# Performance work log

Hardware: AMD Instinct MI355X
Metric: run time of the kernel (lower is better)

Reference implementation:

```python
import jax, jax.numpy as jnp
import numpy as np

N = 16777216  # number of sample points
L = 2         # n_layers


def _layer_unitary(w):
    """U = RZ(w2) @ RY(w1) @ RX(w0), each a standard 2x2 rotation gate."""
    h = w * 0.5
    c, s = jnp.cos(h), jnp.sin(h)
    i = jnp.complex64(1j)
    rx = jnp.array([[1, 0], [0, 1]], jnp.complex64) * c[0] + jnp.array([[0, 1], [1, 0]], jnp.complex64) * (-i * s[0])
    ry = jnp.array([[c[1], -s[1]], [s[1], c[1]]], jnp.complex64)
    rz = jnp.array([[jnp.exp(-i * h[2]), 0.0 + 0.0j], [0.0 + 0.0j, jnp.exp(i * h[2])]], jnp.complex64)
    return rz @ ry @ rx


def setup_inputs() -> dict:
    key = jax.random.key(0)
    k1, k2 = jax.random.split(key)
    x = jax.random.normal(k1, (N, 1), dtype=jnp.float32)
    weights = 0.1 * jax.random.normal(k2, (L, 3), dtype=jnp.float32)
    a = jnp.asarray(1.0, jnp.float32)
    b = jnp.asarray(0.0, jnp.float32)
    return {"x": x, "weights": weights, "a": a, "b": b}


def reference(x, weights, a, b):
    # Total weight-only unitary: product over layers (applied layer 0 first).
    U = jnp.eye(2, dtype=jnp.complex64)
    for l in range(weights.shape[0]):  # static, tiny (L=2)
        U = _layer_unitary(weights[l]) @ U
    # RY(x)|0> = [cos(x/2), sin(x/2)]
    xh = 0.5 * x.reshape(-1)
    state0 = jnp.stack([jnp.cos(xh), jnp.sin(xh)], axis=-1).astype(jnp.complex64)  # [N,2]
    s = jnp.einsum('ij,nj->ni', U, state0)  # [N,2]
    z = (s[:, 0].real ** 2 + s[:, 0].imag ** 2) - (s[:, 1].real ** 2 + s[:, 1].imag ** 2)
    return a * z.reshape(-1, 1) + b
```

## Files before the change

### kernel.cpp

```cpp
#include <hip/hip_runtime.h>


struct cplx { float re, im; };

__device__ inline cplx cmul(cplx p, cplx q) {
    return cplx{p.re * q.re - p.im * q.im, p.re * q.im + p.im * q.re};
}
__device__ inline cplx cadd(cplx p, cplx q) { return cplx{p.re + q.re, p.im + q.im}; }

__device__ inline void qpinn_coeffs(const float* __restrict__ w, float a, float b,
                                    float& K0, float& K1, float& K2) {
    cplx U00{1.f, 0.f}, U01{0.f, 0.f}, U10{0.f, 0.f}, U11{1.f, 0.f};
    #pragma unroll
    for (int l = 0; l < 2; ++l) {
        const float h0 = 0.5f * w[3 * l + 0];
        const float h1 = 0.5f * w[3 * l + 1];
        const float h2 = 0.5f * w[3 * l + 2];
        float c0, s0, c1, s1, c2, s2;
        __sincosf(h0, &s0, &c0);
        __sincosf(h1, &s1, &c1);
        __sincosf(h2, &s2, &c2);

        cplx X00{c0, 0.f}, X01{0.f, -s0}, X10{0.f, -s0}, X11{c0, 0.f};
        cplx Y00{c1, 0.f}, Y01{-s1, 0.f}, Y10{s1, 0.f}, Y11{c1, 0.f};
        cplx A00 = cadd(cmul(Y00, X00), cmul(Y01, X10));
        cplx A01 = cadd(cmul(Y00, X01), cmul(Y01, X11));
        cplx A10 = cadd(cmul(Y10, X00), cmul(Y11, X10));
        cplx A11 = cadd(cmul(Y10, X01), cmul(Y11, X11));
        cplx zm{c2, -s2}, zp{c2, s2};
        cplx L00 = cmul(zm, A00), L01 = cmul(zm, A01);
        cplx L10 = cmul(zp, A10), L11 = cmul(zp, A11);
        cplx n00 = cadd(cmul(L00, U00), cmul(L01, U10));
        cplx n01 = cadd(cmul(L00, U01), cmul(L01, U11));
        cplx n10 = cadd(cmul(L10, U00), cmul(L11, U10));
        cplx n11 = cadd(cmul(L10, U01), cmul(L11, U11));
        U00 = n00; U01 = n01; U10 = n10; U11 = n11;
    }
    const float A = (U00.re * U00.re + U00.im * U00.im) - (U10.re * U10.re + U10.im * U10.im);
    const float B = (U01.re * U01.re + U01.im * U01.im) - (U11.re * U11.re + U11.im * U11.im);
    const float C = 2.f * ((U00.re * U01.re + U00.im * U01.im) -
                           (U10.re * U11.re + U10.im * U11.im));
    K0 = fmaf(a, 0.5f * (A + B), b);
    K1 = a * 0.5f * (A - B);
    K2 = a * 0.5f * C;
}

__global__ __launch_bounds__(256) void qpinn_fused(
    const float* __restrict__ x, const float* __restrict__ w,
    const float* __restrict__ pa, const float* __restrict__ pb,
    float* __restrict__ out, int n4) {

    __shared__ float sc[3];
    if (threadIdx.x == 0) {
        float K0, K1, K2;
        qpinn_coeffs(w, pa[0], pb[0], K0, K1, K2);
        sc[0] = K0; sc[1] = K1; sc[2] = K2;
    }
    __syncthreads();
    const float K0 = sc[0];
    const float K1 = sc[1];
    const float K2 = sc[2];

    const float4* __restrict__ x4 = (const float4*)x;
    float4* __restrict__ o4 = (float4*)out;

    const int stride = gridDim.x * blockDim.x;
    for (int i = blockIdx.x * blockDim.x + threadIdx.x; i < n4; i += stride) {
        float4 v = x4[i];
        float4 r;
        float sx, cx;
        __sincosf(v.x, &sx, &cx); r.x = fmaf(K1, cx, fmaf(K2, sx, K0));
        __sincosf(v.y, &sx, &cx); r.y = fmaf(K1, cx, fmaf(K2, sx, K0));
        __sincosf(v.z, &sx, &cx); r.z = fmaf(K1, cx, fmaf(K2, sx, K0));
        __sincosf(v.w, &sx, &cx); r.w = fmaf(K1, cx, fmaf(K2, sx, K0));
        o4[i] = r;
    }
}

extern "C" void kernel_launch(void* const* d_in, const int* in_sizes, int n_in,
                              void* d_out, int out_size, void* d_ws, size_t ws_size,
                              hipStream_t stream) {
    const float* x = (const float*)d_in[0];
    const float* w = (const float*)d_in[1];
    const float* a = (const float*)d_in[2];
    const float* b = (const float*)d_in[3];
    float* out = (float*)d_out;

    const int n = in_sizes[0];
    const int n4 = n / 4;
    const int block = 256;
    const int grid = 2048;

    qpinn_fused<<<grid, block, 0, stream>>>(x, w, a, b, out, n4);
}
```

Measured before the change: 117.2 us.

## Fold sin/cos combination into single phase-shifted hardware cosine with nontemporal stores

Rewrites K1*cos(x)+K2*sin(x) as R*cos(x - phi), precomputing the amplitude and phase in revolutions so each element needs one v_cos instruction instead of a sincos pair. The grid-stride loop is also unrolled to handle two float4 vectors per iteration, and outputs use nontemporal stores. The kernel is memory-bound at this size, so the main gain would come from fewer ALU ops and better memory-level parallelism. Precision of the raw hardware cosine over larger arguments is a risk.

```diff
diff --git a/kernel.cpp b/kernel.cpp
--- a/kernel.cpp
+++ b/kernel.cpp
@@ -1,5 +1,7 @@
 #include <hip/hip_runtime.h>
 
+
+typedef float f32x4 __attribute__((ext_vector_type(4)));
 
 struct cplx { float re, im; };
 
@@ -9,7 +11,7 @@
 __device__ inline cplx cadd(cplx p, cplx q) { return cplx{p.re + q.re, p.im + q.im}; }
 
 __device__ inline void qpinn_coeffs(const float* __restrict__ w, float a, float b,
-                                    float& K0, float& K1, float& K2) {
+                                    float& K0, float& R, float& mphirev) {
     cplx U00{1.f, 0.f}, U01{0.f, 0.f}, U10{0.f, 0.f}, U11{1.f, 0.f};
     #pragma unroll
     for (int l = 0; l < 2; ++l) {
@@ -17,9 +19,9 @@
         const float h1 = 0.5f * w[3 * l + 1];
         const float h2 = 0.5f * w[3 * l + 2];
         float c0, s0, c1, s1, c2, s2;
-        __sincosf(h0, &s0, &c0);
-        __sincosf(h1, &s1, &c1);
-        __sincosf(h2, &s2, &c2);
+        sincosf(h0, &s0, &c0);
+        sincosf(h1, &s1, &c1);
+        sincosf(h2, &s2, &c2);
 
         cplx X00{c0, 0.f}, X01{0.f, -s0}, X10{0.f, -s0}, X11{c0, 0.f};
         cplx Y00{c1, 0.f}, Y01{-s1, 0.f}, Y10{s1, 0.f}, Y11{c1, 0.f};
@@ -41,8 +43,21 @@
     const float C = 2.f * ((U00.re * U01.re + U00.im * U01.im) -
                            (U10.re * U11.re + U10.im * U11.im));
     K0 = fmaf(a, 0.5f * (A + B), b);
-    K1 = a * 0.5f * (A - B);
-    K2 = a * 0.5f * C;
+    const float K1 = a * 0.5f * (A - B);
+    const float K2 = a * 0.5f * C;
+    R = sqrtf(K1 * K1 + K2 * K2);
+    const float INV2PI = 0.15915494309189535f;
+    mphirev = -atan2f(K2, K1) * INV2PI;
+}
+
+__device__ inline f32x4 qpinn_elem4(f32x4 v, float K0, float R, float mph) {
+    const float INV2PI = 0.15915494309189535f;
+    f32x4 r;
+    r.x = fmaf(R, __builtin_amdgcn_cosf(fmaf(v.x, INV2PI, mph)), K0);
+    r.y = fmaf(R, __builtin_amdgcn_cosf(fmaf(v.y, INV2PI, mph)), K0);
+    r.z = fmaf(R, __builtin_amdgcn_cosf(fmaf(v.z, INV2PI, mph)), K0);
+    r.w = fmaf(R, __builtin_amdgcn_cosf(fmaf(v.w, INV2PI, mph)), K0);
+    return r;
 }
 
 __global__ __launch_bounds__(256) void qpinn_fused(
@@ -52,28 +67,34 @@
 
     __shared__ float sc[3];
     if (threadIdx.x == 0) {
-        float K0, K1, K2;
-        qpinn_coeffs(w, pa[0], pb[0], K0, K1, K2);
-        sc[0] = K0; sc[1] = K1; sc[2] = K2;
+        float K0, R, mph;
+        qpinn_coeffs(w, pa[0], pb[0], K0, R, mph);
+        sc[0] = K0; sc[1] = R; sc[2] = mph;
     }
     __syncthreads();
     const float K0 = sc[0];
-    const float K1 = sc[1];
-    const float K2 = sc[2];
+    const float R  = sc[1];
+    const float mph = sc[2];
 
-    const float4* __restrict__ x4 = (const float4*)x;
-    float4* __restrict__ o4 = (float4*)out;
+    const f32x4* __restrict__ x4 = (const f32x4*)x;
+    f32x4* __restrict__ o4 = (f32x4*)out;
 
     const int stride = gridDim.x * blockDim.x;
-    for (int i = blockIdx.x * blockDim.x + threadIdx.x; i < n4; i += stride) {
-        float4 v = x4[i];
-        float4 r;
-        float sx, cx;
-        __sincosf(v.x, &sx, &cx); r.x = fmaf(K1, cx, fmaf(K2, sx, K0));
-        __sincosf(v.y, &sx, &cx); r.y = fmaf(K1, cx, fmaf(K2, sx, K0));
-        __sincosf(v.z, &sx, &cx); r.z = fmaf(K1, cx, fmaf(K2, sx, K0));
-        __sincosf(v.w, &sx, &cx); r.w = fmaf(K1, cx, fmaf(K2, sx, K0));
-        o4[i] = r;
+    int i = blockIdx.x * blockDim.x + threadIdx.x;
+
+    for (; i + stride < n4; i += 2 * stride) {
+        const int j = i + stride;
+        f32x4 v0 = x4[i];
+        f32x4 v1 = x4[j];
+        f32x4 r0 = qpinn_elem4(v0, K0, R, mph);
+        f32x4 r1 = qpinn_elem4(v1, K0, R, mph);
+        __builtin_nontemporal_store(r0, &o4[i]);
+        __builtin_nontemporal_store(r1, &o4[j]);
+    }
+    if (i < n4) {
+        f32x4 v0 = x4[i];
+        f32x4 r0 = qpinn_elem4(v0, K0, R, mph);
+        __builtin_nontemporal_store(r0, &o4[i]);
     }
 }
 
```

Result: faster. 113.1 us (median of 2 runs) (-3.5%).
